# Kernel tuning notes

Measured on AMD Instinct MI355X. Metric: run time of the kernel, lower is better.

The kernel has to match this reference:

```python
import jax, jax.numpy as jnp
import numpy as np

KERNEL_SIZE = 3
STRIDE = 2

def setup_inputs() -> dict:
    key = jax.random.key(0)
    # Batch of flattened (C,H,W) images; the original flattens to a vector and
    # multiplies by a sparse Toeplitz avg-pool matrix. Equivalent dense-layout input:
    x = jax.random.normal(key, (8, 64, 512, 512), dtype=jnp.float32)
    return {"x": x}

def reference(x):
    # Faithful math of What.dot(x): strided 2D average pooling (VALID windows),
    # applied independently per channel, sum over k x k window divided by k^2.
    k, s = KERNEL_SIZE, STRIDE
    summed = jax.lax.reduce_window(
        x, 0.0, jax.lax.add,
        window_dimensions=(1, 1, k, k),
        window_strides=(1, 1, s, s),
        padding="VALID",
    )
    return summed / jnp.asarray(k * k, dtype=x.dtype)
```

## Files before the change

### kernel.cpp

```cpp
#include <hip/hip_runtime.h>


#define IN_N 8
#define IN_C 64
#define IN_H 512
#define IN_W 512
#define OUT_H 255
#define OUT_W 255

__global__ __launch_bounds__(128) void KeyedAvgpool2d_kernel(
    const float* __restrict__ in, float* __restrict__ out) {
    const int t   = threadIdx.x;
    const int oh  = blockIdx.y;
    const int nc  = blockIdx.z;
    const int ow0 = 2 * t;
    if (ow0 >= OUT_W) return;

    const float* base = in + (size_t)nc * (IN_H * IN_W)
                           + (size_t)(2 * oh) * IN_W
                           + 4 * t;
    float s0 = 0.0f, s1 = 0.0f;
#pragma unroll
    for (int r = 0; r < 3; ++r) {
        const float* row = base + r * IN_W;
        float4 v = *(const float4*)row;
        float  e = row[4];
        s0 += v.x + v.y + v.z;
        s1 += v.z + v.w + e;
    }

    float* orow = out + (size_t)nc * (OUT_H * OUT_W) + (size_t)oh * OUT_W + ow0;
    const float inv9 = 1.0f / 9.0f;
    orow[0] = s0 * inv9;
    if (ow0 + 1 < OUT_W) orow[1] = s1 * inv9;
}

extern "C" void kernel_launch(void* const* d_in, const int* in_sizes, int n_in,
                              void* d_out, int out_size, void* d_ws, size_t ws_size,
                              hipStream_t stream) {
    const float* x = (const float*)d_in[0];
    float* out = (float*)d_out;

    dim3 block(128, 1, 1);
    dim3 grid(1, OUT_H, IN_N * IN_C);
    KeyedAvgpool2d_kernel<<<grid, block, 0, stream>>>(x, out);
}
```

Measured before the change: 704.6 us.

## Compute 2x4 output tile per thread and share overlapping input row

Each thread now produces two output rows by four columns, loading five input rows with two float4 loads each instead of three rows per single output row pair. The shared middle row is reused between the two output rows, reducing redundant input reads, and the grid shrinks to fewer, larger 256-thread blocks. Row indices are clamped at the bottom edge and the last column/row are guarded, adding some branching.

```diff
diff --git a/kernel.cpp b/kernel.cpp
--- a/kernel.cpp
+++ b/kernel.cpp
@@ -1,38 +1,55 @@
 #include <hip/hip_runtime.h>
 
 
-#define IN_N 8
-#define IN_C 64
 #define IN_H 512
 #define IN_W 512
 #define OUT_H 255
 #define OUT_W 255
+#define PLANES 512
 
-__global__ __launch_bounds__(128) void KeyedAvgpool2d_kernel(
+__global__ __launch_bounds__(256) void KeyedAvgpool2d_kernel(
     const float* __restrict__ in, float* __restrict__ out) {
-    const int t   = threadIdx.x;
-    const int oh  = blockIdx.y;
-    const int nc  = blockIdx.z;
-    const int ow0 = 2 * t;
-    if (ow0 >= OUT_W) return;
+    const int tid = threadIdx.x;
+    const int t   = tid & 63;
+    const int g   = tid >> 6;
+    const int p   = blockIdx.x * 4 + g;
+    const int nc  = blockIdx.y;
+    const int oh0 = 2 * p;
+    const bool has2 = (oh0 + 1) < OUT_H;
 
-    const float* base = in + (size_t)nc * (IN_H * IN_W)
-                           + (size_t)(2 * oh) * IN_W
-                           + 4 * t;
-    float s0 = 0.0f, s1 = 0.0f;
+    const float* plane = in + (size_t)nc * (IN_H * IN_W);
+
+    float a00 = 0, a01 = 0, a02 = 0, a03 = 0;
+    float a10 = 0, a11 = 0, a12 = 0, a13 = 0;
 #pragma unroll
-    for (int r = 0; r < 3; ++r) {
-        const float* row = base + r * IN_W;
-        float4 v = *(const float4*)row;
-        float  e = row[4];
-        s0 += v.x + v.y + v.z;
-        s1 += v.z + v.w + e;
+    for (int r = 0; r < 5; ++r) {
+        int ir = 2 * oh0 + r;
+        ir = ir > (IN_H - 1) ? (IN_H - 1) : ir;
+        const float* row = plane + (size_t)ir * IN_W + 8 * t;
+        float4 v0 = *(const float4*)row;
+        float4 v1 = *(const float4*)(row + 4);
+        float  c8 = (t < 63) ? row[8] : 0.0f;
+        float h0 = v0.x + v0.y + v0.z;
+        float h1 = v0.z + v0.w + v1.x;
+        float h2 = v1.x + v1.y + v1.z;
+        float h3 = v1.z + v1.w + c8;
+        if (r < 3)  { a00 += h0; a01 += h1; a02 += h2; a03 += h3; }
+        if (r >= 2) { a10 += h0; a11 += h1; a12 += h2; a13 += h3; }
     }
 
-    float* orow = out + (size_t)nc * (OUT_H * OUT_W) + (size_t)oh * OUT_W + ow0;
     const float inv9 = 1.0f / 9.0f;
-    orow[0] = s0 * inv9;
-    if (ow0 + 1 < OUT_W) orow[1] = s1 * inv9;
+    float* o0 = out + (size_t)nc * (OUT_H * OUT_W) + (size_t)oh0 * OUT_W + 4 * t;
+    o0[0] = a00 * inv9;
+    o0[1] = a01 * inv9;
+    o0[2] = a02 * inv9;
+    if (t < 63) o0[3] = a03 * inv9;
+    if (has2) {
+        float* o1 = o0 + OUT_W;
+        o1[0] = a10 * inv9;
+        o1[1] = a11 * inv9;
+        o1[2] = a12 * inv9;
+        if (t < 63) o1[3] = a13 * inv9;
+    }
 }
 
 extern "C" void kernel_launch(void* const* d_in, const int* in_sizes, int n_in,
@@ -41,7 +58,7 @@
     const float* x = (const float*)d_in[0];
     float* out = (float*)d_out;
 
-    dim3 block(128, 1, 1);
-    dim3 grid(1, OUT_H, IN_N * IN_C);
+    dim3 block(256, 1, 1);
+    dim3 grid(32, PLANES, 1);
     KeyedAvgpool2d_kernel<<<grid, block, 0, stream>>>(x, out);
 }
```

New measurement: 703.8 us. No clear change (-0.1%).
